# Optimization experiments

Measured on AMD Instinct MI355X. Metric: run time of the kernel, lower is better.

## Reference

```python
import jax, jax.numpy as jnp
import numpy as np
from jax import lax


def setup_inputs() -> dict:
    key = jax.random.key(0)
    I = jax.random.uniform(key, (32, 3, 512, 512), dtype=jnp.float32)
    return {"I": I, "k": 15}


def reference(I, k):
    # Channel-wise min -> dark channel (torch does this via -max_pool over transposed channel dim)
    dark = jnp.min(I, axis=1, keepdims=True)  # [B,1,H,W]
    p = k // 2
    # Spatial min-pool kxk, stride 1, pad k//2. torch max_pool2d pads with -inf,
    # so the min-pool equivalent pads with +inf: reduce_window with min and +inf init.
    eroded = lax.reduce_window(
        dark,
        jnp.inf,
        lax.min,
        window_dimensions=(1, 1, k, k),
        window_strides=(1, 1, 1, 1),
        padding=[(0, 0), (0, 0), (p, p), (p, p)],
    )
    return eroded
```

## Files before the change

kernel.cpp:

```cpp
#include <hip/hip_runtime.h>
#include <math.h>

#define BATCH 32
#define CH    3
#define H     512
#define W     512
#define KWIN  15
#define PAD   7
#define T2    16

static __device__ __forceinline__ float2 min2(float2 a, float2 b) {
    float2 r;
    r.x = fminf(a.x, b.x);
    r.y = fminf(a.y, b.y);
    return r;
}

__global__ void dcp_p1(const float* __restrict__ I, float* __restrict__ tmp) {
    const int bh = blockIdx.x;
    const int b  = bh >> 9;
    const int h  = bh & (H - 1);
    const int t  = threadIdx.x;
    const int x  = t * 2;

    __shared__ float s[W + 2 * PAD + 2];

    const float* p = I + ((size_t)b * CH * H + h) * W + x;
    const float2 a0 = *(const float2*)(p);
    const float2 a1 = *(const float2*)(p + (size_t)H * W);
    const float2 a2 = *(const float2*)(p + (size_t)2 * H * W);
    const float2 d  = min2(min2(a0, a1), a2);
    s[PAD + x]     = d.x;
    s[PAD + x + 1] = d.y;
    if (t < PAD) {
        s[t]           = INFINITY;
        s[PAD + W + t] = INFINITY;
    }
    __syncthreads();

    float2 w[8];
    #pragma unroll
    for (int j = 0; j < 8; ++j) w[j] = *(const float2*)&s[x + 2 * j];
    float m = fminf(w[0].y, w[7].x);
    #pragma unroll
    for (int j = 1; j < 7; ++j) m = fminf(m, fminf(w[j].x, w[j].y));
    float2 o;
    o.x = fminf(m, w[0].x);
    o.y = fminf(m, w[7].y);
    *(float2*)(tmp + ((size_t)b * H + h) * W + x) = o;
}

__global__ void dcp_p2(const float* __restrict__ tmp, float* __restrict__ out) {
    const int x  = threadIdx.x * 2;
    const int y0 = blockIdx.x * T2;
    const int b  = blockIdx.y;

    const float* col = tmp + (size_t)b * H * W + x;
    float*       o   = out + (size_t)b * H * W + x;

    float2 vb[KWIN];
    #pragma unroll
    for (int j = 0; j < KWIN; ++j) {
        const int y = min(y0 + 8 + j, H - 1);
        vb[j] = *(const float2*)(col + (size_t)y * W);
    }
    if (y0 + 8 + KWIN - 1 >= H) {
        const float2 inf2 = make_float2(INFINITY, INFINITY);
        #pragma unroll
        for (int j = 0; j < KWIN; ++j)
            if (y0 + 8 + j >= H) vb[j] = inf2;
    }
    float2 P[KWIN];
    P[0] = vb[0];
    #pragma unroll
    for (int j = 1; j < KWIN; ++j) P[j] = min2(P[j - 1], vb[j]);
    *(float2*)(o + (size_t)(y0 + 15) * W) = P[14];

    float2 va[KWIN];
    #pragma unroll
    for (int i = 0; i < KWIN; ++i) {
        const int y = max(y0 - PAD + i, 0);
        va[i] = *(const float2*)(col + (size_t)y * W);
    }
    if (y0 == 0) {
        const float2 inf2 = make_float2(INFINITY, INFINITY);
        #pragma unroll
        for (int i = 0; i < PAD; ++i) va[i] = inf2;
    }
    float2 run = va[14];
    *(float2*)(o + (size_t)(y0 + 14) * W) = min2(run, P[13]);
    #pragma unroll
    for (int r = 13; r >= 1; --r) {
        run = min2(run, va[r]);
        *(float2*)(o + (size_t)(y0 + r) * W) = min2(run, P[r - 1]);
    }
    run = min2(run, va[0]);
    *(float2*)(o + (size_t)y0 * W) = run;
}

extern "C" void kernel_launch(void* const* d_in, const int* in_sizes, int n_in,
                              void* d_out, int out_size, void* d_ws, size_t ws_size,
                              hipStream_t stream) {
    const float* I = (const float*)d_in[0];
    float* out = (float*)d_out;
    float* tmp = (float*)d_ws;

    dcp_p1<<<dim3(BATCH * H), dim3(256), 0, stream>>>(I, tmp);
    dcp_p2<<<dim3(H / T2, BATCH), dim3(256), 0, stream>>>(tmp, out);
}
```

Baseline: 166.4 us.

## Replace shared-memory row min-pool with per-wavefront shuffle prefix/suffix scan

The horizontal min pass now assigns one row to each 64-lane wavefront, with each lane owning 8 contiguous pixels loaded as float4 pairs. Neighbouring lanes exchange prefix and suffix minima through cross-lane shuffles, replacing the LDS staging buffer and the __syncthreads barrier. The 15-wide window is built from its own block minimum plus the neighbours' partial minima, and blocks shrink fourfold in count. This trades LDS traffic for 14 shuffles per lane and more registers. It also assumes a 64-wide wavefront, so the 512-pixel row maps exactly onto one wavefront.

Result: no change. 167.4 us (+0.6%).

```diff
diff --git a/kernel.cpp b/kernel.cpp
--- a/kernel.cpp
+++ b/kernel.cpp
@@ -15,39 +15,70 @@
     r.y = fminf(a.y, b.y);
     return r;
 }
+static __device__ __forceinline__ float4 min4(float4 a, float4 b) {
+    float4 r;
+    r.x = fminf(a.x, b.x); r.y = fminf(a.y, b.y);
+    r.z = fminf(a.z, b.z); r.w = fminf(a.w, b.w);
+    return r;
+}
 
 __global__ void dcp_p1(const float* __restrict__ I, float* __restrict__ tmp) {
-    const int bh = blockIdx.x;
-    const int b  = bh >> 9;
-    const int h  = bh & (H - 1);
-    const int t  = threadIdx.x;
-    const int x  = t * 2;
-
-    __shared__ float s[W + 2 * PAD + 2];
+    const int wid = (blockIdx.x << 2) + (threadIdx.x >> 6);
+    const int b   = wid >> 9;
+    const int h   = wid & (H - 1);
+    const int L   = threadIdx.x & 63;
+    const int x   = L * 8;
 
     const float* p = I + ((size_t)b * CH * H + h) * W + x;
-    const float2 a0 = *(const float2*)(p);
-    const float2 a1 = *(const float2*)(p + (size_t)H * W);
-    const float2 a2 = *(const float2*)(p + (size_t)2 * H * W);
-    const float2 d  = min2(min2(a0, a1), a2);
-    s[PAD + x]     = d.x;
-    s[PAD + x + 1] = d.y;
-    if (t < PAD) {
-        s[t]           = INFINITY;
-        s[PAD + W + t] = INFINITY;
+    const float4 a0 = *(const float4*)(p);
+    const float4 a1 = *(const float4*)(p + 4);
+    const float4 b0 = *(const float4*)(p + (size_t)H * W);
+    const float4 b1 = *(const float4*)(p + (size_t)H * W + 4);
+    const float4 c0 = *(const float4*)(p + (size_t)2 * H * W);
+    const float4 c1 = *(const float4*)(p + (size_t)2 * H * W + 4);
+
+    const float4 mlo = min4(min4(a0, b0), c0);
+    const float4 mhi = min4(min4(a1, b1), c1);
+    const float m0 = mlo.x, m1 = mlo.y, m2 = mlo.z, m3 = mlo.w;
+    const float m4 = mhi.x, m5 = mhi.y, m6 = mhi.z, m7 = mhi.w;
+
+    float pr[8], sf[8];
+    pr[0] = m0; pr[1] = fminf(pr[0], m1); pr[2] = fminf(pr[1], m2);
+    pr[3] = fminf(pr[2], m3); pr[4] = fminf(pr[3], m4); pr[5] = fminf(pr[4], m5);
+    pr[6] = fminf(pr[5], m6); pr[7] = fminf(pr[6], m7);
+    sf[7] = m7; sf[6] = fminf(m6, sf[7]); sf[5] = fminf(m5, sf[6]);
+    sf[4] = fminf(m4, sf[5]); sf[3] = fminf(m3, sf[4]); sf[2] = fminf(m2, sf[3]);
+    sf[1] = fminf(m1, sf[2]); sf[0] = fminf(m0, sf[1]);
+    const float M = pr[7];
+
+    float sl[7], pn[7];
+    #pragma unroll
+    for (int j = 0; j < 7; ++j) {
+        sl[j] = __shfl_up(sf[j + 1], 1);
+        pn[j] = __shfl_down(pr[j], 1);
     }
-    __syncthreads();
+    if (L == 0) {
+        #pragma unroll
+        for (int j = 0; j < 7; ++j) sl[j] = INFINITY;
+    }
+    if (L == 63) {
+        #pragma unroll
+        for (int j = 0; j < 7; ++j) pn[j] = INFINITY;
+    }
 
-    float2 w[8];
-    #pragma unroll
-    for (int j = 0; j < 8; ++j) w[j] = *(const float2*)&s[x + 2 * j];
-    float m = fminf(w[0].y, w[7].x);
-    #pragma unroll
-    for (int j = 1; j < 7; ++j) m = fminf(m, fminf(w[j].x, w[j].y));
-    float2 o;
-    o.x = fminf(m, w[0].x);
-    o.y = fminf(m, w[7].y);
-    *(float2*)(tmp + ((size_t)b * H + h) * W + x) = o;
+    float4 olo, ohi;
+    olo.x = fminf(M, sl[0]);
+    olo.y = fminf(M, fminf(sl[1], pn[0]));
+    olo.z = fminf(M, fminf(sl[2], pn[1]));
+    olo.w = fminf(M, fminf(sl[3], pn[2]));
+    ohi.x = fminf(M, fminf(sl[4], pn[3]));
+    ohi.y = fminf(M, fminf(sl[5], pn[4]));
+    ohi.z = fminf(M, fminf(sl[6], pn[5]));
+    ohi.w = fminf(M, pn[6]);
+
+    float* q = tmp + ((size_t)b * H + h) * W + x;
+    *(float4*)(q)     = olo;
+    *(float4*)(q + 4) = ohi;
 }
 
 __global__ void dcp_p2(const float* __restrict__ tmp, float* __restrict__ out) {
@@ -105,6 +136,6 @@
     float* out = (float*)d_out;
     float* tmp = (float*)d_ws;
 
-    dcp_p1<<<dim3(BATCH * H), dim3(256), 0, stream>>>(I, tmp);
+    dcp_p1<<<dim3((BATCH * H) / 4), dim3(256), 0, stream>>>(I, tmp);
     dcp_p2<<<dim3(H / T2, BATCH), dim3(256), 0, stream>>>(tmp, out);
 }
```
